# Kernel tuning notes

Hardware: AMD Instinct MI355X
Metric: run time of the kernel (lower is better)

The kernel has to match this reference:

```python
import jax, jax.numpy as jnp
import numpy as np

B, S, D = 8, 2048, 128
H = 4
HD = D // H  # 32


def setup_inputs() -> dict:
    key = jax.random.key(0)
    k1, k2, k3 = jax.random.split(key, 3)
    x = jax.random.normal(k1, (B, S, D), dtype=jnp.float32)
    w_attn = jax.random.normal(k2, (D, 3 * D), dtype=jnp.float32) * (1.0 / np.sqrt(D))
    w_proj = jax.random.normal(k3, (D, D), dtype=jnp.float32) * (1.0 / np.sqrt(D))
    return {"x": x, "w_attn": w_attn, "w_proj": w_proj}


def reference(x, w_attn, w_proj):
    b, s, d = x.shape
    qkv = x @ w_attn  # [B,S,3D]
    q, k, v = jnp.split(qkv, 3, axis=-1)
    # [B,H,S,HD]
    q = q.reshape(b, s, H, HD).transpose(0, 2, 1, 3)
    k = k.reshape(b, s, H, HD).transpose(0, 2, 1, 3)
    v = v.reshape(b, s, H, HD).transpose(0, 2, 1, 3)
    scale = 1.0 / jnp.sqrt(jnp.asarray(HD, dtype=x.dtype))
    scores = jnp.einsum('bhqd,bhkd->bhqk', q, k) * scale  # [B,H,S,S]
    causal = jnp.tril(jnp.ones((s, s), dtype=bool))
    scores = jnp.where(causal, scores, jnp.finfo(x.dtype).min)
    attn = jax.nn.softmax(scores, axis=-1)
    out = jnp.einsum('bhqk,bhkd->bhqd', attn, v)  # [B,H,S,HD]
    out = out.transpose(0, 2, 1, 3).reshape(b, s, d)
    out = out @ w_proj  # c_proj; dropout is identity in eval
    return out
```

## Files before the change

kernel.cpp:

```cpp
#include <hip/hip_runtime.h>
#include <hip/hip_bf16.h>

#define B_  8
#define S_  2048
#define D_  128
#define H_  4
#define HD_ 32
#define BH_ (B_ * H_)

typedef __bf16 bf16x8 __attribute__((ext_vector_type(8)));
typedef float f32x16 __attribute__((ext_vector_type(16)));

__device__ inline bf16x8 ld8(const __hip_bfloat16* p) {
    return *reinterpret_cast<const bf16x8*>(p);
}
__device__ inline unsigned cvtpk(float lo, float hi) {
    unsigned r;
    asm("v_cvt_pk_bf16_f32 %0, %1, %2" : "=v"(r) : "v"(lo), "v"(hi));
    return r;
}
__device__ inline void swap32(unsigned &a, unsigned &b) {
    asm("v_permlane32_swap_b32 %0, %1" : "+v"(a), "+v"(b));
}
__device__ inline float ex2(float x) { return __builtin_amdgcn_exp2f(x); }

__global__ __launch_bounds__(256) void qkv_mfma(const float* __restrict__ x,
                                                const float* __restrict__ wa,
                                                __hip_bfloat16* __restrict__ Qb,
                                                __hip_bfloat16* __restrict__ Kb,
                                                __hip_bfloat16* __restrict__ Vt) {
    __shared__ __align__(16) __hip_bfloat16 wl[96][136];

    const int head = blockIdx.x & 3;
    const int mblk = blockIdx.x >> 2;
    const int tid  = threadIdx.x;

    for (int idx = tid; idx < 128 * 96; idx += 256) {
        const int k = idx / 96;
        const int c = idx - k * 96;
        const int sec = c >> 5, nloc = c & 31;
        wl[c][k] = __float2bfloat16(wa[k * 384 + sec * 128 + head * 32 + nloc]);
    }
    __syncthreads();

    const int wave = tid >> 6;
    const int lane = tid & 63;
    const int lq   = lane & 31;
    const int hi   = lane >> 5;
    const int m0   = mblk * 128 + wave * 32;

    const float* ax = x + (m0 + lq) * 128 + 8 * hi;
    const __hip_bfloat16* bq = &wl[lq][8 * hi];
    const __hip_bfloat16* bk = &wl[32 + lq][8 * hi];
    const __hip_bfloat16* bv = &wl[64 + lq][8 * hi];

    f32x16 aq = {}, ak = {}, av = {};
#pragma unroll
    for (int ks = 0; ks < 8; ++ks) {
        float4 x0 = *reinterpret_cast<const float4*>(ax + 16 * ks);
        float4 x1 = *reinterpret_cast<const float4*>(ax + 16 * ks + 4);
        union { unsigned u[4]; bf16x8 v; } af;
        af.u[0] = cvtpk(x0.x, x0.y); af.u[1] = cvtpk(x0.z, x0.w);
        af.u[2] = cvtpk(x1.x, x1.y); af.u[3] = cvtpk(x1.z, x1.w);
        const bf16x8 wqf = ld8(bq + 16 * ks);
        const bf16x8 wkf = ld8(bk + 16 * ks);
        const bf16x8 wvf = ld8(bv + 16 * ks);
        aq = __builtin_amdgcn_mfma_f32_32x32x16_bf16(wqf, af.v, aq, 0, 0, 0);
        ak = __builtin_amdgcn_mfma_f32_32x32x16_bf16(wkf, af.v, ak, 0, 0, 0);
        av = __builtin_amdgcn_mfma_f32_32x32x16_bf16(af.v, wvf, av, 0, 0, 0);
    }

    const int b  = m0 >> 11;
    const int s0 = m0 & (S_ - 1);
    const int bh = b * H_ + head;
    const float qs = 0.2550052557342824f;

    __hip_bfloat16* qrow = Qb + (bh * S_ + s0 + lq) * HD_ + 4 * hi;
    __hip_bfloat16* krow = Kb + (bh * S_ + s0 + lq) * HD_ + 4 * hi;
#pragma unroll
    for (int g = 0; g < 4; ++g) {
        union { __hip_bfloat16 h[4]; ushort4 u; } pq, pk;
#pragma unroll
        for (int j = 0; j < 4; ++j) {
            pq.h[j] = __float2bfloat16(aq[4 * g + j] * qs);
            pk.h[j] = __float2bfloat16(ak[4 * g + j]);
        }
        *reinterpret_cast<ushort4*>(qrow + 8 * g) = pq.u;
        *reinterpret_cast<ushort4*>(krow + 8 * g) = pk.u;
    }
    __hip_bfloat16* vbase = Vt + (bh * HD_ + lq) * S_ + s0;
#pragma unroll
    for (int g = 0; g < 4; ++g) {
        union { __hip_bfloat16 h[4]; ushort4 u; } pv;
#pragma unroll
        for (int j = 0; j < 4; ++j) pv.h[j] = __float2bfloat16(av[4 * g + j]);
        *reinterpret_cast<ushort4*>(vbase + 8 * g + 4 * hi) = pv.u;
    }
}

__global__ __launch_bounds__(256, 4) void fattn_kernel(
    const __hip_bfloat16* __restrict__ Qb,
    const __hip_bfloat16* __restrict__ Kb,
    const __hip_bfloat16* __restrict__ Vt,
    __hip_bfloat16* __restrict__ AOb)
{
    __shared__ float Ol[4][64][33];
    __shared__ float Ll[4][64];

    const int bh   = blockIdx.x & 31;
    const int qt2  = 31 - (blockIdx.x >> 5);
    const int tid  = threadIdx.x;
    const int wv   = tid >> 6;
    const int lane = tid & 63;
    const int lq   = lane & 31;
    const int hi   = lane >> 5;

    const int q0  = qt2 * 64;
    const int qtA = 2 * qt2;
    const int qtB = qtA + 1;
    const int nt  = qtB + 1;

    const __hip_bfloat16* qrowA = Qb + (bh * S_ + q0 + lq) * HD_ + 8 * hi;
    const __hip_bfloat16* qrowB = qrowA + 32 * HD_;
    const bf16x8 qfA0 = ld8(qrowA), qfA1 = ld8(qrowA + 16);
    const bf16x8 qfB0 = ld8(qrowB), qfB1 = ld8(qrowB + 16);

    const __hip_bfloat16* kp = Kb + bh * S_ * HD_ + lq * HD_ + 8 * hi;
    const __hip_bfloat16* vp = Vt + (bh * HD_ + lq) * S_ + 8 * hi;

    f32x16 oaccA = {}, oaccB = {};
    float lsumA = 0.f, lsumB = 0.f;

    bf16x8 k0a = {}, k1a = {}, v0a = {}, v1a = {};
    if (wv < nt) {
        k0a = ld8(kp + wv * 32 * HD_); k1a = ld8(kp + wv * 32 * HD_ + 16);
        v0a = ld8(vp + wv * 32);       v1a = ld8(vp + wv * 32 + 16);
    }

    for (int t = wv; t < nt; t += 4) {
        const bf16x8 ck0 = k0a, ck1 = k1a, cv0 = v0a, cv1 = v1a;
        if (t + 4 < nt) {
            const __hip_bfloat16* kn = kp + (t + 4) * 32 * HD_;
            const __hip_bfloat16* vn = vp + (t + 4) * 32;
            k0a = ld8(kn); k1a = ld8(kn + 16);
            v0a = ld8(vn); v1a = ld8(vn + 16);
        }

        if (t <= qtA) {
            __builtin_amdgcn_s_setprio(1);
            f32x16 s = {};
            s = __builtin_amdgcn_mfma_f32_32x32x16_bf16(ck0, qfA0, s, 0, 0, 0);
            s = __builtin_amdgcn_mfma_f32_32x32x16_bf16(ck1, qfA1, s, 0, 0, 0);
            __builtin_amdgcn_s_setprio(0);

            if (t == qtA) {
#pragma unroll
                for (int r = 0; r < 16; ++r) {
                    const int kloc = (r & 3) + 8 * (r >> 2) + 4 * hi;
                    s[r] = (kloc > lq) ? -1e30f : s[r];
                }
            }
#pragma unroll
            for (int r = 0; r < 16; ++r) s[r] = ex2(s[r]);
            {
                float p0 = (s[0] + s[1]) + (s[2] + s[3]);
                float p1 = (s[4] + s[5]) + (s[6] + s[7]);
                float p2 = (s[8] + s[9]) + (s[10] + s[11]);
                float p3 = (s[12] + s[13]) + (s[14] + s[15]);
                lsumA += (p0 + p1) + (p2 + p3);
            }
            unsigned a0 = cvtpk(s[0], s[1]),   a1 = cvtpk(s[2], s[3]);
            unsigned a2 = cvtpk(s[4], s[5]),   a3 = cvtpk(s[6], s[7]);
            swap32(a0, a2); swap32(a1, a3);
            unsigned b0 = cvtpk(s[8], s[9]),   b1 = cvtpk(s[10], s[11]);
            unsigned b2 = cvtpk(s[12], s[13]), b3 = cvtpk(s[14], s[15]);
            swap32(b0, b2); swap32(b1, b3);
            union { unsigned u[4]; bf16x8 v; } pb0, pb1;
            pb0.u[0] = a0; pb0.u[1] = a1; pb0.u[2] = a2; pb0.u[3] = a3;
            pb1.u[0] = b0; pb1.u[1] = b1; pb1.u[2] = b2; pb1.u[3] = b3;

            __builtin_amdgcn_s_setprio(1);
            oaccA = __builtin_amdgcn_mfma_f32_32x32x16_bf16(cv0, pb0.v, oaccA, 0, 0, 0);
            oaccA = __builtin_amdgcn_mfma_f32_32x32x16_bf16(cv1, pb1.v, oaccA, 0, 0, 0);
            __builtin_amdgcn_s_setprio(0);
        }

        {
            __builtin_amdgcn_s_setprio(1);
            f32x16 s = {};
            s = __builtin_amdgcn_mfma_f32_32x32x16_bf16(ck0, qfB0, s, 0, 0, 0);
            s = __builtin_amdgcn_mfma_f32_32x32x16_bf16(ck1, qfB1, s, 0, 0, 0);
            __builtin_amdgcn_s_setprio(0);

            if (t == qtB) {
#pragma unroll
                for (int r = 0; r < 16; ++r) {
                    const int kloc = (r & 3) + 8 * (r >> 2) + 4 * hi;
                    s[r] = (kloc > lq) ? -1e30f : s[r];
                }
            }
#pragma unroll
            for (int r = 0; r < 16; ++r) s[r] = ex2(s[r]);
            {
                float p0 = (s[0] + s[1]) + (s[2] + s[3]);
                float p1 = (s[4] + s[5]) + (s[6] + s[7]);
                float p2 = (s[8] + s[9]) + (s[10] + s[11]);
                float p3 = (s[12] + s[13]) + (s[14] + s[15]);
                lsumB += (p0 + p1) + (p2 + p3);
            }
            unsigned a0 = cvtpk(s[0], s[1]),   a1 = cvtpk(s[2], s[3]);
            unsigned a2 = cvtpk(s[4], s[5]),   a3 = cvtpk(s[6], s[7]);
            swap32(a0, a2); swap32(a1, a3);
            unsigned b0 = cvtpk(s[8], s[9]),   b1 = cvtpk(s[10], s[11]);
            unsigned b2 = cvtpk(s[12], s[13]), b3 = cvtpk(s[14], s[15]);
            swap32(b0, b2); swap32(b1, b3);
            union { unsigned u[4]; bf16x8 v; } pb0, pb1;
            pb0.u[0] = a0; pb0.u[1] = a1; pb0.u[2] = a2; pb0.u[3] = a3;
            pb1.u[0] = b0; pb1.u[1] = b1; pb1.u[2] = b2; pb1.u[3] = b3;

            __builtin_amdgcn_s_setprio(1);
            oaccB = __builtin_amdgcn_mfma_f32_32x32x16_bf16(cv0, pb0.v, oaccB, 0, 0, 0);
            oaccB = __builtin_amdgcn_mfma_f32_32x32x16_bf16(cv1, pb1.v, oaccB, 0, 0, 0);
            __builtin_amdgcn_s_setprio(0);
        }
    }

    lsumA += __shfl_xor(lsumA, 32);
    lsumB += __shfl_xor(lsumB, 32);

#pragma unroll
    for (int r = 0; r < 16; ++r) {
        const int d = (r & 3) + 8 * (r >> 2) + 4 * hi;
        Ol[wv][lq][d]      = oaccA[r];
        Ol[wv][32 + lq][d] = oaccB[r];
    }
    if (hi == 0) { Ll[wv][lq] = lsumA; Ll[wv][32 + lq] = lsumB; }
    __syncthreads();

    const int q  = tid >> 2;
    const int d0 = (tid & 3) * 8;
    const float lst = Ll[0][q] + Ll[1][q] + Ll[2][q] + Ll[3][q];
    const float inv = 1.f / lst;

    const int b = bh >> 2, h = bh & 3;
    __hip_bfloat16* orow = AOb + (b * S_ + q0 + q) * D_ + h * HD_ + d0;
#pragma unroll
    for (int g = 0; g < 2; ++g) {
        union { __hip_bfloat16 h4[4]; ushort4 u; } st;
#pragma unroll
        for (int j = 0; j < 4; ++j) {
            const int d = d0 + 4 * g + j;
            const float o = Ol[0][q][d] + Ol[1][q][d] + Ol[2][q][d] + Ol[3][q][d];
            st.h4[j] = __float2bfloat16(o * inv);
        }
        *reinterpret_cast<ushort4*>(orow + 4 * g) = st.u;
    }
}

__global__ __launch_bounds__(256) void proj_mfma(const __hip_bfloat16* __restrict__ AOb,
                                                 const float* __restrict__ wp,
                                                 float* __restrict__ out) {
    __shared__ __align__(16) __hip_bfloat16 wl[128][136];

    const int tid = threadIdx.x;
    for (int idx = tid; idx < 128 * 128; idx += 256) {
        const int k = idx >> 7, n = idx & 127;
        wl[n][k] = __float2bfloat16(wp[idx]);
    }
    __syncthreads();

    const int m0   = blockIdx.x * 32;
    const int wave = tid >> 6;
    const int lane = tid & 63;
    const int lq   = lane & 31;
    const int hi   = lane >> 5;
    const int n0   = wave * 32;

    const __hip_bfloat16* ap = AOb + (m0 + lq) * 128 + 8 * hi;
    const __hip_bfloat16* bp = &wl[n0 + lq][8 * hi];

    f32x16 acc = {};
#pragma unroll
    for (int ks = 0; ks < 8; ++ks) {
        const bf16x8 af = ld8(ap + 16 * ks);
        const bf16x8 bf = ld8(bp + 16 * ks);
        acc = __builtin_amdgcn_mfma_f32_32x32x16_bf16(bf, af, acc, 0, 0, 0);
    }

    float* orow = out + (m0 + lq) * 128 + n0 + 4 * hi;
#pragma unroll
    for (int g = 0; g < 4; ++g) {
        float4 st = make_float4(acc[4 * g], acc[4 * g + 1], acc[4 * g + 2], acc[4 * g + 3]);
        *reinterpret_cast<float4*>(orow + 8 * g) = st;
    }
}

extern "C" void kernel_launch(void* const* d_in, const int* in_sizes, int n_in,
                              void* d_out, int out_size, void* d_ws, size_t ws_size,
                              hipStream_t stream) {
    const float* x      = (const float*)d_in[0];
    const float* w_attn = (const float*)d_in[1];
    const float* w_proj = (const float*)d_in[2];
    float* out = (float*)d_out;

    char* ws = (char*)d_ws;
    __hip_bfloat16* Qb  = (__hip_bfloat16*)(ws);
    __hip_bfloat16* Kb  = (__hip_bfloat16*)(ws + (4  << 20));
    __hip_bfloat16* Vt  = (__hip_bfloat16*)(ws + (8  << 20));
    __hip_bfloat16* AOb = (__hip_bfloat16*)(ws + (12 << 20));

    qkv_mfma<<<512, 256, 0, stream>>>(x, w_attn, Qb, Kb, Vt);
    fattn_kernel<<<BH_ * 32, 256, 0, stream>>>(Qb, Kb, Vt, AOb);
    proj_mfma<<<512, 256, 0, stream>>>(AOb, w_proj, out);
}
```

Baseline: 47.08 us.

## Fuse output projection into attention epilogue with per-head atomic accumulation

Removes the separate projection kernel. Each attention block now multiplies its normalized per-head output tile by that head's 32-row slice of w_proj and atomically adds the fp32 result into the output. The QKV kernel zeroes the output beforehand. This saves a launch and the bf16 attention-output round trip through global memory, but adds four-way float atomics per output element and a w_proj load into LDS in every attention block.

```diff
diff --git a/kernel.cpp b/kernel.cpp
--- a/kernel.cpp
+++ b/kernel.cpp
@@ -28,12 +28,20 @@
                                                 const float* __restrict__ wa,
                                                 __hip_bfloat16* __restrict__ Qb,
                                                 __hip_bfloat16* __restrict__ Kb,
-                                                __hip_bfloat16* __restrict__ Vt) {
+                                                __hip_bfloat16* __restrict__ Vt,
+                                                float* __restrict__ out) {
     __shared__ __align__(16) __hip_bfloat16 wl[96][136];
 
     const int head = blockIdx.x & 3;
     const int mblk = blockIdx.x >> 2;
     const int tid  = threadIdx.x;
+
+    {
+        float4 z4 = make_float4(0.f, 0.f, 0.f, 0.f);
+        float4* zp = reinterpret_cast<float4*>(out + (mblk * 128 + head * 32) * 128);
+#pragma unroll
+        for (int i = 0; i < 4; ++i) zp[tid + 256 * i] = z4;
+    }
 
     for (int idx = tid; idx < 128 * 96; idx += 256) {
         const int k = idx / 96;
@@ -102,10 +110,13 @@
     const __hip_bfloat16* __restrict__ Qb,
     const __hip_bfloat16* __restrict__ Kb,
     const __hip_bfloat16* __restrict__ Vt,
-    __hip_bfloat16* __restrict__ AOb)
+    const float* __restrict__ wp,
+    float* __restrict__ out)
 {
     __shared__ float Ol[4][64][33];
     __shared__ float Ll[4][64];
+    __shared__ __align__(16) __hip_bfloat16 Osm[64][40];
+    __shared__ __align__(16) __hip_bfloat16 wpl[128][40];
 
     const int bh   = blockIdx.x & 31;
     const int qt2  = 31 - (blockIdx.x >> 5);
@@ -114,6 +125,12 @@
     const int lane = tid & 63;
     const int lq   = lane & 31;
     const int hi   = lane >> 5;
+    const int h    = bh & 3;
+
+    for (int idx = tid; idx < 128 * 32; idx += 256) {
+        const int k = idx >> 7, n = idx & 127;
+        wpl[n][k] = __float2bfloat16(wp[(h * 32 + k) * 128 + n]);
+    }
 
     const int q0  = qt2 * 64;
     const int qtA = 2 * qt2;
@@ -237,61 +254,43 @@
     if (hi == 0) { Ll[wv][lq] = lsumA; Ll[wv][32 + lq] = lsumB; }
     __syncthreads();
 
-    const int q  = tid >> 2;
-    const int d0 = (tid & 3) * 8;
-    const float lst = Ll[0][q] + Ll[1][q] + Ll[2][q] + Ll[3][q];
-    const float inv = 1.f / lst;
-
-    const int b = bh >> 2, h = bh & 3;
-    __hip_bfloat16* orow = AOb + (b * S_ + q0 + q) * D_ + h * HD_ + d0;
-#pragma unroll
-    for (int g = 0; g < 2; ++g) {
-        union { __hip_bfloat16 h4[4]; ushort4 u; } st;
-#pragma unroll
-        for (int j = 0; j < 4; ++j) {
-            const int d = d0 + 4 * g + j;
-            const float o = Ol[0][q][d] + Ol[1][q][d] + Ol[2][q][d] + Ol[3][q][d];
-            st.h4[j] = __float2bfloat16(o * inv);
-        }
-        *reinterpret_cast<ushort4*>(orow + 4 * g) = st.u;
-    }
-}
-
-__global__ __launch_bounds__(256) void proj_mfma(const __hip_bfloat16* __restrict__ AOb,
-                                                 const float* __restrict__ wp,
-                                                 float* __restrict__ out) {
-    __shared__ __align__(16) __hip_bfloat16 wl[128][136];
-
-    const int tid = threadIdx.x;
-    for (int idx = tid; idx < 128 * 128; idx += 256) {
-        const int k = idx >> 7, n = idx & 127;
-        wl[n][k] = __float2bfloat16(wp[idx]);
+    {
+        const int q  = tid >> 2;
+        const int d0 = (tid & 3) * 8;
+        const float lst = Ll[0][q] + Ll[1][q] + Ll[2][q] + Ll[3][q];
+        const float inv = 1.f / lst;
+#pragma unroll
+        for (int g = 0; g < 2; ++g) {
+            union { __hip_bfloat16 h4[4]; ushort4 u; } st;
+#pragma unroll
+            for (int j = 0; j < 4; ++j) {
+                const int d = d0 + 4 * g + j;
+                const float o = Ol[0][q][d] + Ol[1][q][d] + Ol[2][q][d] + Ol[3][q][d];
+                st.h4[j] = __float2bfloat16(o * inv);
+            }
+            *reinterpret_cast<ushort4*>(&Osm[q][d0 + 4 * g]) = st.u;
+        }
     }
     __syncthreads();
 
-    const int m0   = blockIdx.x * 32;
-    const int wave = tid >> 6;
-    const int lane = tid & 63;
-    const int lq   = lane & 31;
-    const int hi   = lane >> 5;
-    const int n0   = wave * 32;
-
-    const __hip_bfloat16* ap = AOb + (m0 + lq) * 128 + 8 * hi;
-    const __hip_bfloat16* bp = &wl[n0 + lq][8 * hi];
-
-    f32x16 acc = {};
-#pragma unroll
-    for (int ks = 0; ks < 8; ++ks) {
-        const bf16x8 af = ld8(ap + 16 * ks);
-        const bf16x8 bf = ld8(bp + 16 * ks);
-        acc = __builtin_amdgcn_mfma_f32_32x32x16_bf16(bf, af, acc, 0, 0, 0);
-    }
-
-    float* orow = out + (m0 + lq) * 128 + n0 + 4 * hi;
-#pragma unroll
-    for (int g = 0; g < 4; ++g) {
-        float4 st = make_float4(acc[4 * g], acc[4 * g + 1], acc[4 * g + 2], acc[4 * g + 3]);
-        *reinterpret_cast<float4*>(orow + 8 * g) = st;
+    {
+        const int b = bh >> 2;
+        const bf16x8 wf0 = ld8(&wpl[wv * 32 + lq][8 * hi]);
+        const bf16x8 wf1 = ld8(&wpl[wv * 32 + lq][16 + 8 * hi]);
+#pragma unroll
+        for (int mt = 0; mt < 2; ++mt) {
+            const bf16x8 of0 = ld8(&Osm[mt * 32 + lq][8 * hi]);
+            const bf16x8 of1 = ld8(&Osm[mt * 32 + lq][16 + 8 * hi]);
+            f32x16 acc = {};
+            acc = __builtin_amdgcn_mfma_f32_32x32x16_bf16(of0, wf0, acc, 0, 0, 0);
+            acc = __builtin_amdgcn_mfma_f32_32x32x16_bf16(of1, wf1, acc, 0, 0, 0);
+            float* obase = out + (b * S_ + q0 + mt * 32) * 128 + wv * 32 + lq;
+#pragma unroll
+            for (int r = 0; r < 16; ++r) {
+                const int row = (r & 3) + 8 * (r >> 2) + 4 * hi;
+                atomicAdd(obase + row * 128, acc[r]);
+            }
+        }
     }
 }
 
@@ -304,12 +303,10 @@
     float* out = (float*)d_out;
 
     char* ws = (char*)d_ws;
-    __hip_bfloat16* Qb  = (__hip_bfloat16*)(ws);
-    __hip_bfloat16* Kb  = (__hip_bfloat16*)(ws + (4  << 20));
-    __hip_bfloat16* Vt  = (__hip_bfloat16*)(ws + (8  << 20));
-    __hip_bfloat16* AOb = (__hip_bfloat16*)(ws + (12 << 20));
-
-    qkv_mfma<<<512, 256, 0, stream>>>(x, w_attn, Qb, Kb, Vt);
-    fattn_kernel<<<BH_ * 32, 256, 0, stream>>>(Qb, Kb, Vt, AOb);
-    proj_mfma<<<512, 256, 0, stream>>>(AOb, w_proj, out);
-}
+    __hip_bfloat16* Qb = (__hip_bfloat16*)(ws);
+    __hip_bfloat16* Kb = (__hip_bfloat16*)(ws + (4 << 20));
+    __hip_bfloat16* Vt = (__hip_bfloat16*)(ws + (8 << 20));
+
+    qkv_mfma<<<512, 256, 0, stream>>>(x, w_attn, Qb, Kb, Vt, out);
+    fattn_kernel<<<BH_ * 32, 256, 0, stream>>>(Qb, Kb, Vt, w_proj, out);
+}
```

After: 63.88 us. 35.7% more time.

## Unroll attention key loop by two tiles with independent accumulators

Applied to the files above, without the earlier changes.

The key/value tile loop now handles two tiles per iteration, stride 8 instead of 4. Each query half gets two independent output accumulators and row-sum partials, so the MFMA and exp chains of the two tiles can interleave and hide dependency latency. The partials are summed before the shared-memory reduction. Diagonal masking is generalised to a per-tile limit, so the A-half now computes the fully masked tile qtB as zeros instead of skipping it. Launch bounds drop from 4 to 3 waves per SIMD to leave room for the extra registers, at the cost of occupancy.

```diff
diff --git a/kernel.cpp b/kernel.cpp
--- a/kernel.cpp
+++ b/kernel.cpp
@@ -98,7 +98,7 @@
     }
 }
 
-__global__ __launch_bounds__(256, 4) void fattn_kernel(
+__global__ __launch_bounds__(256, 3) void fattn_kernel(
     const __hip_bfloat16* __restrict__ Qb,
     const __hip_bfloat16* __restrict__ Kb,
     const __hip_bfloat16* __restrict__ Vt,
@@ -128,111 +128,89 @@
     const __hip_bfloat16* kp = Kb + bh * S_ * HD_ + lq * HD_ + 8 * hi;
     const __hip_bfloat16* vp = Vt + (bh * HD_ + lq) * S_ + 8 * hi;
 
-    f32x16 oaccA = {}, oaccB = {};
-    float lsumA = 0.f, lsumB = 0.f;
-
-    bf16x8 k0a = {}, k1a = {}, v0a = {}, v1a = {};
+    f32x16 oA1 = {}, oA2 = {}, oB1 = {}, oB2 = {};
+    float lA1 = 0.f, lA2 = 0.f, lB1 = 0.f, lB2 = 0.f;
+
+    bf16x8 kA0 = {}, kA1 = {}, vA0 = {}, vA1 = {};
     if (wv < nt) {
-        k0a = ld8(kp + wv * 32 * HD_); k1a = ld8(kp + wv * 32 * HD_ + 16);
-        v0a = ld8(vp + wv * 32);       v1a = ld8(vp + wv * 32 + 16);
-    }
-
-    for (int t = wv; t < nt; t += 4) {
-        const bf16x8 ck0 = k0a, ck1 = k1a, cv0 = v0a, cv1 = v1a;
-        if (t + 4 < nt) {
+        kA0 = ld8(kp + wv * 32 * HD_); kA1 = ld8(kp + wv * 32 * HD_ + 16);
+        vA0 = ld8(vp + wv * 32);       vA1 = ld8(vp + wv * 32 + 16);
+    }
+
+#define TILEWORK(T, QF0, QF1, DT, CK0, CK1, CV0, CV1, OACC, LS)                 \
+    {                                                                           \
+        __builtin_amdgcn_s_setprio(1);                                          \
+        f32x16 s = {};                                                          \
+        s = __builtin_amdgcn_mfma_f32_32x32x16_bf16(CK0, QF0, s, 0, 0, 0);      \
+        s = __builtin_amdgcn_mfma_f32_32x32x16_bf16(CK1, QF1, s, 0, 0, 0);      \
+        __builtin_amdgcn_s_setprio(0);                                          \
+        if ((T) >= (DT)) {                                                      \
+            const int lim = lq + (((DT) - (T)) << 5);                           \
+            _Pragma("unroll")                                                   \
+            for (int r = 0; r < 16; ++r) {                                      \
+                const int kloc = (r & 3) + 8 * (r >> 2) + 4 * hi;               \
+                s[r] = (kloc > lim) ? -1e30f : s[r];                            \
+            }                                                                   \
+        }                                                                       \
+        _Pragma("unroll")                                                       \
+        for (int r = 0; r < 16; ++r) s[r] = ex2(s[r]);                          \
+        {                                                                       \
+            float p0 = (s[0] + s[1]) + (s[2] + s[3]);                           \
+            float p1 = (s[4] + s[5]) + (s[6] + s[7]);                           \
+            float p2 = (s[8] + s[9]) + (s[10] + s[11]);                         \
+            float p3 = (s[12] + s[13]) + (s[14] + s[15]);                       \
+            LS += (p0 + p1) + (p2 + p3);                                        \
+        }                                                                       \
+        unsigned a0 = cvtpk(s[0], s[1]),   a1 = cvtpk(s[2], s[3]);              \
+        unsigned a2 = cvtpk(s[4], s[5]),   a3 = cvtpk(s[6], s[7]);              \
+        swap32(a0, a2); swap32(a1, a3);                                         \
+        unsigned b0 = cvtpk(s[8], s[9]),   b1 = cvtpk(s[10], s[11]);            \
+        unsigned b2 = cvtpk(s[12], s[13]), b3 = cvtpk(s[14], s[15]);            \
+        swap32(b0, b2); swap32(b1, b3);                                         \
+        union { unsigned u[4]; bf16x8 v; } pb0, pb1;                            \
+        pb0.u[0] = a0; pb0.u[1] = a1; pb0.u[2] = a2; pb0.u[3] = a3;             \
+        pb1.u[0] = b0; pb1.u[1] = b1; pb1.u[2] = b2; pb1.u[3] = b3;             \
+        __builtin_amdgcn_s_setprio(1);                                          \
+        OACC = __builtin_amdgcn_mfma_f32_32x32x16_bf16(CV0, pb0.v, OACC, 0, 0, 0); \
+        OACC = __builtin_amdgcn_mfma_f32_32x32x16_bf16(CV1, pb1.v, OACC, 0, 0, 0); \
+        __builtin_amdgcn_s_setprio(0);                                          \
+    }
+
+    for (int t = wv; t < nt; t += 8) {
+        const bf16x8 cka0 = kA0, cka1 = kA1, cva0 = vA0, cva1 = vA1;
+        const bool odd = (t + 4 < nt);
+
+        bf16x8 ckb0 = {}, ckb1 = {}, cvb0 = {}, cvb1 = {};
+        if (odd) {
             const __hip_bfloat16* kn = kp + (t + 4) * 32 * HD_;
             const __hip_bfloat16* vn = vp + (t + 4) * 32;
-            k0a = ld8(kn); k1a = ld8(kn + 16);
-            v0a = ld8(vn); v1a = ld8(vn + 16);
-        }
-
-        if (t <= qtA) {
-            __builtin_amdgcn_s_setprio(1);
-            f32x16 s = {};
-            s = __builtin_amdgcn_mfma_f32_32x32x16_bf16(ck0, qfA0, s, 0, 0, 0);
-            s = __builtin_amdgcn_mfma_f32_32x32x16_bf16(ck1, qfA1, s, 0, 0, 0);
-            __builtin_amdgcn_s_setprio(0);
-
-            if (t == qtA) {
-#pragma unroll
-                for (int r = 0; r < 16; ++r) {
-                    const int kloc = (r & 3) + 8 * (r >> 2) + 4 * hi;
-                    s[r] = (kloc > lq) ? -1e30f : s[r];
-                }
-            }
-#pragma unroll
-            for (int r = 0; r < 16; ++r) s[r] = ex2(s[r]);
-            {
-                float p0 = (s[0] + s[1]) + (s[2] + s[3]);
-                float p1 = (s[4] + s[5]) + (s[6] + s[7]);
-                float p2 = (s[8] + s[9]) + (s[10] + s[11]);
-                float p3 = (s[12] + s[13]) + (s[14] + s[15]);
-                lsumA += (p0 + p1) + (p2 + p3);
-            }
-            unsigned a0 = cvtpk(s[0], s[1]),   a1 = cvtpk(s[2], s[3]);
-            unsigned a2 = cvtpk(s[4], s[5]),   a3 = cvtpk(s[6], s[7]);
-            swap32(a0, a2); swap32(a1, a3);
-            unsigned b0 = cvtpk(s[8], s[9]),   b1 = cvtpk(s[10], s[11]);
-            unsigned b2 = cvtpk(s[12], s[13]), b3 = cvtpk(s[14], s[15]);
-            swap32(b0, b2); swap32(b1, b3);
-            union { unsigned u[4]; bf16x8 v; } pb0, pb1;
-            pb0.u[0] = a0; pb0.u[1] = a1; pb0.u[2] = a2; pb0.u[3] = a3;
-            pb1.u[0] = b0; pb1.u[1] = b1; pb1.u[2] = b2; pb1.u[3] = b3;
-
-            __builtin_amdgcn_s_setprio(1);
-            oaccA = __builtin_amdgcn_mfma_f32_32x32x16_bf16(cv0, pb0.v, oaccA, 0, 0, 0);
-            oaccA = __builtin_amdgcn_mfma_f32_32x32x16_bf16(cv1, pb1.v, oaccA, 0, 0, 0);
-            __builtin_amdgcn_s_setprio(0);
-        }
-
-        {
-            __builtin_amdgcn_s_setprio(1);
-            f32x16 s = {};
-            s = __builtin_amdgcn_mfma_f32_32x32x16_bf16(ck0, qfB0, s, 0, 0, 0);
-            s = __builtin_amdgcn_mfma_f32_32x32x16_bf16(ck1, qfB1, s, 0, 0, 0);
-            __builtin_amdgcn_s_setprio(0);
-
-            if (t == qtB) {
-#pragma unroll
-                for (int r = 0; r < 16; ++r) {
-                    const int kloc = (r & 3) + 8 * (r >> 2) + 4 * hi;
-                    s[r] = (kloc > lq) ? -1e30f : s[r];
-                }
-            }
-#pragma unroll
-            for (int r = 0; r < 16; ++r) s[r] = ex2(s[r]);
-            {
-                float p0 = (s[0] + s[1]) + (s[2] + s[3]);
-                float p1 = (s[4] + s[5]) + (s[6] + s[7]);
-                float p2 = (s[8] + s[9]) + (s[10] + s[11]);
-                float p3 = (s[12] + s[13]) + (s[14] + s[15]);
-                lsumB += (p0 + p1) + (p2 + p3);
-            }
-            unsigned a0 = cvtpk(s[0], s[1]),   a1 = cvtpk(s[2], s[3]);
-            unsigned a2 = cvtpk(s[4], s[5]),   a3 = cvtpk(s[6], s[7]);
-            swap32(a0, a2); swap32(a1, a3);
-            unsigned b0 = cvtpk(s[8], s[9]),   b1 = cvtpk(s[10], s[11]);
-            unsigned b2 = cvtpk(s[12], s[13]), b3 = cvtpk(s[14], s[15]);
-            swap32(b0, b2); swap32(b1, b3);
-            union { unsigned u[4]; bf16x8 v; } pb0, pb1;
-            pb0.u[0] = a0; pb0.u[1] = a1; pb0.u[2] = a2; pb0.u[3] = a3;
-            pb1.u[0] = b0; pb1.u[1] = b1; pb1.u[2] = b2; pb1.u[3] = b3;
-
-            __builtin_amdgcn_s_setprio(1);
-            oaccB = __builtin_amdgcn_mfma_f32_32x32x16_bf16(cv0, pb0.v, oaccB, 0, 0, 0);
-            oaccB = __builtin_amdgcn_mfma_f32_32x32x16_bf16(cv1, pb1.v, oaccB, 0, 0, 0);
-            __builtin_amdgcn_s_setprio(0);
-        }
-    }
-
+            ckb0 = ld8(kn); ckb1 = ld8(kn + 16);
+            cvb0 = ld8(vn); cvb1 = ld8(vn + 16);
+        }
+        if (t + 8 < nt) {
+            const __hip_bfloat16* kn = kp + (t + 8) * 32 * HD_;
+            const __hip_bfloat16* vn = vp + (t + 8) * 32;
+            kA0 = ld8(kn); kA1 = ld8(kn + 16);
+            vA0 = ld8(vn); vA1 = ld8(vn + 16);
+        }
+
+        TILEWORK(t, qfA0, qfA1, qtA, cka0, cka1, cva0, cva1, oA1, lA1)
+        if (odd) TILEWORK(t + 4, qfA0, qfA1, qtA, ckb0, ckb1, cvb0, cvb1, oA2, lA2)
+        TILEWORK(t, qfB0, qfB1, qtB, cka0, cka1, cva0, cva1, oB1, lB1)
+        if (odd) TILEWORK(t + 4, qfB0, qfB1, qtB, ckb0, ckb1, cvb0, cvb1, oB2, lB2)
+    }
+#undef TILEWORK
+
+    float lsumA = lA1 + lA2;
+    float lsumB = lB1 + lB2;
     lsumA += __shfl_xor(lsumA, 32);
     lsumB += __shfl_xor(lsumB, 32);
 
 #pragma unroll
     for (int r = 0; r < 16; ++r) {
         const int d = (r & 3) + 8 * (r >> 2) + 4 * hi;
-        Ol[wv][lq][d]      = oaccA[r];
-        Ol[wv][32 + lq][d] = oaccB[r];
+        Ol[wv][lq][d]      = oA1[r] + oA2[r];
+        Ol[wv][32 + lq][d] = oB1[r] + oB2[r];
     }
     if (hi == 0) { Ll[wv][lq] = lsumA; Ll[wv][32 + lq] = lsumB; }
     __syncthreads();
```

New measurement: 72.23 us. 1.53x slower.

## Store K and V in MFMA fragment-native tiled layout for coalesced loads

Applied to the files above, without the earlier changes.

The QKV projection now writes K and V tiles of 32 keys in a packed layout matching the per-lane MFMA fragment order, so each 32-key tile is a contiguous 2KB block. The attention kernel then loads K and V fragments as fully contiguous lane*8 reads instead of strided row/column accesses. This is meant to cut memory transactions and improve coalescing in the attention inner loop. The V fragment layout also changes from a transposed store to the same tiled store as K, which must still match the operand order the MFMAs expect.

```diff
diff --git a/kernel.cpp b/kernel.cpp
--- a/kernel.cpp
+++ b/kernel.cpp
@@ -27,8 +27,8 @@
 __global__ __launch_bounds__(256) void qkv_mfma(const float* __restrict__ x,
                                                 const float* __restrict__ wa,
                                                 __hip_bfloat16* __restrict__ Qb,
-                                                __hip_bfloat16* __restrict__ Kb,
-                                                __hip_bfloat16* __restrict__ Vt) {
+                                                __hip_bfloat16* __restrict__ Kf,
+                                                __hip_bfloat16* __restrict__ Vf) {
     __shared__ __align__(16) __hip_bfloat16 wl[96][136];
 
     const int head = blockIdx.x & 3;
@@ -73,35 +73,32 @@
     const int b  = m0 >> 11;
     const int s0 = m0 & (S_ - 1);
     const int bh = b * H_ + head;
+    const int t  = s0 >> 5;
     const float qs = 0.2550052557342824f;
 
     __hip_bfloat16* qrow = Qb + (bh * S_ + s0 + lq) * HD_ + 4 * hi;
-    __hip_bfloat16* krow = Kb + (bh * S_ + s0 + lq) * HD_ + 4 * hi;
+    __hip_bfloat16* kfb  = Kf + ((bh * 64 + t) << 10);
+    __hip_bfloat16* vfb  = Vf + ((bh * 64 + t) << 10);
 #pragma unroll
     for (int g = 0; g < 4; ++g) {
-        union { __hip_bfloat16 h[4]; ushort4 u; } pq, pk;
+        union { __hip_bfloat16 h[4]; ushort4 u; } pq, pk, pv;
 #pragma unroll
         for (int j = 0; j < 4; ++j) {
             pq.h[j] = __float2bfloat16(aq[4 * g + j] * qs);
             pk.h[j] = __float2bfloat16(ak[4 * g + j]);
+            pv.h[j] = __float2bfloat16(av[4 * g + j]);
         }
         *reinterpret_cast<ushort4*>(qrow + 8 * g) = pq.u;
-        *reinterpret_cast<ushort4*>(krow + 8 * g) = pk.u;
-    }
-    __hip_bfloat16* vbase = Vt + (bh * HD_ + lq) * S_ + s0;
-#pragma unroll
-    for (int g = 0; g < 4; ++g) {
-        union { __hip_bfloat16 h[4]; ushort4 u; } pv;
-#pragma unroll
-        for (int j = 0; j < 4; ++j) pv.h[j] = __float2bfloat16(av[4 * g + j]);
-        *reinterpret_cast<ushort4*>(vbase + 8 * g + 4 * hi) = pv.u;
+        const int off = ((g >> 1) << 9) + ((((g & 1) << 5) + lq) << 3) + 4 * hi;
+        *reinterpret_cast<ushort4*>(kfb + off) = pk.u;
+        *reinterpret_cast<ushort4*>(vfb + off) = pv.u;
     }
 }
 
 __global__ __launch_bounds__(256, 4) void fattn_kernel(
     const __hip_bfloat16* __restrict__ Qb,
-    const __hip_bfloat16* __restrict__ Kb,
-    const __hip_bfloat16* __restrict__ Vt,
+    const __hip_bfloat16* __restrict__ Kf,
+    const __hip_bfloat16* __restrict__ Vf,
     __hip_bfloat16* __restrict__ AOb)
 {
     __shared__ float Ol[4][64][33];
@@ -125,25 +122,23 @@
     const bf16x8 qfA0 = ld8(qrowA), qfA1 = ld8(qrowA + 16);
     const bf16x8 qfB0 = ld8(qrowB), qfB1 = ld8(qrowB + 16);
 
-    const __hip_bfloat16* kp = Kb + bh * S_ * HD_ + lq * HD_ + 8 * hi;
-    const __hip_bfloat16* vp = Vt + (bh * HD_ + lq) * S_ + 8 * hi;
+    const __hip_bfloat16* kp = Kf + (bh << 16) + lane * 8;
+    const __hip_bfloat16* vp = Vf + (bh << 16) + lane * 8;
 
     f32x16 oaccA = {}, oaccB = {};
     float lsumA = 0.f, lsumB = 0.f;
 
     bf16x8 k0a = {}, k1a = {}, v0a = {}, v1a = {};
     if (wv < nt) {
-        k0a = ld8(kp + wv * 32 * HD_); k1a = ld8(kp + wv * 32 * HD_ + 16);
-        v0a = ld8(vp + wv * 32);       v1a = ld8(vp + wv * 32 + 16);
+        k0a = ld8(kp + wv * 1024); k1a = ld8(kp + wv * 1024 + 512);
+        v0a = ld8(vp + wv * 1024); v1a = ld8(vp + wv * 1024 + 512);
     }
 
     for (int t = wv; t < nt; t += 4) {
         const bf16x8 ck0 = k0a, ck1 = k1a, cv0 = v0a, cv1 = v1a;
         if (t + 4 < nt) {
-            const __hip_bfloat16* kn = kp + (t + 4) * 32 * HD_;
-            const __hip_bfloat16* vn = vp + (t + 4) * 32;
-            k0a = ld8(kn); k1a = ld8(kn + 16);
-            v0a = ld8(vn); v1a = ld8(vn + 16);
+            k0a = ld8(kp + (t + 4) * 1024); k1a = ld8(kp + (t + 4) * 1024 + 512);
+            v0a = ld8(vp + (t + 4) * 1024); v1a = ld8(vp + (t + 4) * 1024 + 512);
         }
 
         if (t <= qtA) {
@@ -305,11 +300,11 @@
 
     char* ws = (char*)d_ws;
     __hip_bfloat16* Qb  = (__hip_bfloat16*)(ws);
-    __hip_bfloat16* Kb  = (__hip_bfloat16*)(ws + (4  << 20));
-    __hip_bfloat16* Vt  = (__hip_bfloat16*)(ws + (8  << 20));
+    __hip_bfloat16* Kf  = (__hip_bfloat16*)(ws + (4  << 20));
+    __hip_bfloat16* Vf  = (__hip_bfloat16*)(ws + (8  << 20));
     __hip_bfloat16* AOb = (__hip_bfloat16*)(ws + (12 << 20));
 
-    qkv_mfma<<<512, 256, 0, stream>>>(x, w_attn, Qb, Kb, Vt);
-    fattn_kernel<<<BH_ * 32, 256, 0, stream>>>(Qb, Kb, Vt, AOb);
+    qkv_mfma<<<512, 256, 0, stream>>>(x, w_attn, Qb, Kf, Vf);
+    fattn_kernel<<<BH_ * 32, 256, 0, stream>>>(Qb, Kf, Vf, AOb);
     proj_mfma<<<512, 256, 0, stream>>>(AOb, w_proj, out);
 }
```

After: 42.76 us (median of 2 runs). 9.2% less time.
